# Performance work log

Hardware: AMD Instinct MI355X
Metric: run time of the kernel (lower is better)

Reference implementation:

```python
import jax, jax.numpy as jnp
import numpy as np

N_HEADS = 16
EPS = 1e-4


def setup_inputs() -> dict:
    key = jax.random.key(0)
    ks = jax.random.split(key, 9)
    B, L, E = 4, 4096, 1024
    s = 1.0 / np.sqrt(E)
    return {
        "x": jax.random.normal(ks[0], (B, L, E), dtype=jnp.float32),
        "Wq": jax.random.normal(ks[1], (E, E), dtype=jnp.float32) * s,
        "bq": jax.random.normal(ks[2], (E,), dtype=jnp.float32) * 0.01,
        "Wk": jax.random.normal(ks[3], (E, E), dtype=jnp.float32) * s,
        "bk": jax.random.normal(ks[4], (E,), dtype=jnp.float32) * 0.01,
        "Wv": jax.random.normal(ks[5], (E, E), dtype=jnp.float32) * s,
        "bv": jax.random.normal(ks[6], (E,), dtype=jnp.float32) * 0.01,
        "Wo": jax.random.normal(ks[7], (E, E), dtype=jnp.float32) * s,
        "bo": jax.random.normal(ks[8], (E,), dtype=jnp.float32) * 0.01,
    }


def _cosformer(x, Wq, bq, Wk, bk, Wv, bv, Wo, bo):
    B, L, E = x.shape
    H = N_HEADS
    hd = E // H
    # torch Linear: y = x @ W.T + b; self-attention so q=k=v source is x
    q = jax.nn.relu(jnp.einsum('ble,fe->blf', x, Wq) + bq)
    k = jax.nn.relu(jnp.einsum('ble,fe->blf', x, Wk) + bk)
    v = jnp.einsum('ble,fe->blf', x, Wv) + bv
    # (B, L, E) -> (B*H, L, hd)  [matches torch view(L, B*H, hd).transpose(0,1)]
    def split_heads(t):
        return t.reshape(B, L, H, hd).transpose(0, 2, 1, 3).reshape(B * H, L, hd)
    q, k, v = split_heads(q), split_heads(k), split_heads(v)
    m = L  # src_len == tgt_len
    idx = (np.pi / 2) * jnp.arange(1, m + 1, dtype=jnp.float32) / m  # (m,)
    sin = jnp.sin(idx)[None, :, None]
    cos = jnp.cos(idx)[None, :, None]
    q_ = jnp.concatenate([q * sin, q * cos], axis=-1)  # (BH, L, 2hd)
    k_ = jnp.concatenate([k * sin, k * cos], axis=-1)
    kv = jnp.einsum('nld,nlm->ndm', k_, v)             # (BH, 2hd, hd)
    z = 1.0 / jnp.maximum(jnp.einsum('nld,nd->nl', q_, k_.sum(axis=1)), EPS)
    attn = jnp.einsum('nld,ndm->nlm', q_, kv) * z[:, :, None]  # (BH, L, hd)
    # (B*H, L, hd) -> (B, L, E)
    out = attn.reshape(B, H, L, hd).transpose(0, 2, 1, 3).reshape(B, L, E)
    return jnp.einsum('ble,fe->blf', out, Wo) + bo


def reference(x, Wq, bq, Wk, bk, Wv, bv, Wo, bo):
    return _cosformer(x, Wq, bq, Wk, bk, Wv, bv, Wo, bo)
```

## Files before the change

### kernel.cpp

```cpp
#include <hip/hip_runtime.h>


typedef unsigned short u16;
typedef unsigned int u32;
typedef __attribute__((ext_vector_type(8))) __bf16 bf16x8;
typedef __attribute__((ext_vector_type(4))) float f32x4;

#define PI_HALF 1.57079632679489662f
#define EPS_Z 1e-4f

__device__ __forceinline__ u16 f32_to_bf16(float f) {
    union { float f; unsigned int u; } x; x.f = f;
    unsigned int lsb = (x.u >> 16) & 1u;
    x.u += 0x7fffu + lsb;
    return (u16)(x.u >> 16);
}
__device__ __forceinline__ float bf16_to_f32(u16 u) {
    union { float f; unsigned int u; } x; x.u = ((unsigned int)u) << 16;
    return x.f;
}

typedef __attribute__((address_space(1))) void amdgpu_global_t;
typedef __attribute__((address_space(3))) void amdgpu_lds_t;
__device__ __forceinline__ void async_load16(const u16* g, u16* l) {
    __builtin_amdgcn_global_load_lds((amdgpu_global_t*)g, (amdgpu_lds_t*)l, 16, 0, 0);
}

__global__ __launch_bounds__(256) void cvt_bf16(const float* __restrict__ in,
                                                u16* __restrict__ out, int n4) {
    int i = blockIdx.x * 256 + threadIdx.x;
    if (i >= n4) return;
    float4 f = ((const float4*)in)[i];
    ushort4 o;
    o.x = f32_to_bf16(f.x); o.y = f32_to_bf16(f.y);
    o.z = f32_to_bf16(f.z); o.w = f32_to_bf16(f.w);
    ((ushort4*)out)[i] = o;
}

__global__ __launch_bounds__(256) void cvt_w4(const float* __restrict__ w0,
                                              const float* __restrict__ w1,
                                              const float* __restrict__ w2,
                                              const float* __restrict__ w3,
                                              u16* __restrict__ wcat) {
    const float* src = (blockIdx.y == 0) ? w0 : (blockIdx.y == 1) ? w1
                     : (blockIdx.y == 2) ? w2 : w3;
    u16* dst = wcat + (size_t)blockIdx.y * 1048576;
    int i = blockIdx.x * 256 + threadIdx.x;
    float4 f = ((const float4*)src)[i];
    ushort4 o;
    o.x = f32_to_bf16(f.x); o.y = f32_to_bf16(f.y);
    o.z = f32_to_bf16(f.z); o.w = f32_to_bf16(f.w);
    ((ushort4*)dst)[i] = o;
}

__global__ __launch_bounds__(256) void gemm_qkv(const u16* __restrict__ A,
                                                const u16* __restrict__ Wcat,
                                                const float* __restrict__ bq,
                                                const float* __restrict__ bk,
                                                const float* __restrict__ bv,
                                                u16* __restrict__ qo,
                                                u16* __restrict__ ko,
                                                u16* __restrict__ vo) {
    __shared__ u16 As[128 * 32];
    __shared__ u16 Bs[128 * 32];
    const int K = 1024;
    const int tid  = threadIdx.x;
    const int wave = tid >> 6;
    const int lane = tid & 63;
    const int quad = lane >> 4;
    const int l15  = lane & 15;
    const long tileM = (long)blockIdx.x * 128;
    const long tileN = (long)blockIdx.y * 128;
    const int mat = blockIdx.y >> 3;
    const float* bias = (mat == 0) ? bq : (mat == 1) ? bk : bv;
    u16* outp = (mat == 0) ? qo : (mat == 1) ? ko : vo;
    const bool relu = (mat < 2);
    const int wm = (wave >> 1) * 64;
    const int wn = (wave & 1) * 64;
    const int s_row = wave * 32 + (lane >> 2);
    const int s_col = (lane & 3) * 8;

    const u16* gA = A    + (tileM + s_row) * (long)K + s_col;
    const u16* gB = Wcat + (tileN + s_row) * (long)K + s_col;
    u16* lA = &As[wave * 1024];
    u16* lB = &Bs[wave * 1024];

    f32x4 acc[4][4] = {};

    for (int kb = 0; kb < K; kb += 32) {
        async_load16(gA,                lA);
        async_load16(gA + 16 * (long)K, lA + 512);
        async_load16(gB,                lB);
        async_load16(gB + 16 * (long)K, lB + 512);
        gA += 32; gB += 32;
        __syncthreads();
        bf16x8 af[4], bf[4];
#pragma unroll
        for (int i = 0; i < 4; i++) {
            af[i] = *(const bf16x8*)&As[(wm + i * 16 + l15) * 32 + quad * 8];
            bf[i] = *(const bf16x8*)&Bs[(wn + i * 16 + l15) * 32 + quad * 8];
        }
#pragma unroll
        for (int i = 0; i < 4; i++)
#pragma unroll
            for (int j = 0; j < 4; j++)
                acc[i][j] = __builtin_amdgcn_mfma_f32_16x16x32_bf16(
                    af[i], bf[j], acc[i][j], 0, 0, 0);
        __syncthreads();
    }

#pragma unroll
    for (int j = 0; j < 4; j++) {
        const long n = tileN + wn + j * 16 + l15;
        const int nl = (int)n & 1023;
        const float bv_ = bias[nl];
#pragma unroll
        for (int i = 0; i < 4; i++) {
            const long m0 = tileM + wm + i * 16 + quad * 4;
#pragma unroll
            for (int r = 0; r < 4; r++) {
                float v = acc[i][j][r] + bv_;
                if (relu) v = fmaxf(v, 0.0f);
                outp[(m0 + r) * 1024 + nl] = f32_to_bf16(v);
            }
        }
    }
}

__global__ __launch_bounds__(256) void gemm_o(const u16* __restrict__ A,
                                              const u16* __restrict__ Bw,
                                              const float* __restrict__ bias,
                                              float* __restrict__ Cout,
                                              int M, int N, int K) {
    __shared__ u16 As[128 * 32];
    __shared__ u16 Bs[128 * 32];
    const int tid  = threadIdx.x;
    const int wave = tid >> 6;
    const int lane = tid & 63;
    const int quad = lane >> 4;
    const int l15  = lane & 15;
    const long tileM = (long)blockIdx.x * 128;
    const long tileN = (long)blockIdx.y * 128;
    const int wm = (wave >> 1) * 64;
    const int wn = (wave & 1) * 64;
    const int s_row = wave * 32 + (lane >> 2);
    const int s_col = (lane & 3) * 8;

    const u16* gA = A  + (tileM + s_row) * (long)K + s_col;
    const u16* gB = Bw + (tileN + s_row) * (long)K + s_col;
    u16* lA = &As[wave * 1024];
    u16* lB = &Bs[wave * 1024];

    f32x4 acc[4][4] = {};

    for (int kb = 0; kb < K; kb += 32) {
        async_load16(gA,                lA);
        async_load16(gA + 16 * (long)K, lA + 512);
        async_load16(gB,                lB);
        async_load16(gB + 16 * (long)K, lB + 512);
        gA += 32; gB += 32;
        __syncthreads();
        bf16x8 af[4], bf[4];
#pragma unroll
        for (int i = 0; i < 4; i++) {
            af[i] = *(const bf16x8*)&As[(wm + i * 16 + l15) * 32 + quad * 8];
            bf[i] = *(const bf16x8*)&Bs[(wn + i * 16 + l15) * 32 + quad * 8];
        }
#pragma unroll
        for (int i = 0; i < 4; i++)
#pragma unroll
            for (int j = 0; j < 4; j++)
                acc[i][j] = __builtin_amdgcn_mfma_f32_16x16x32_bf16(
                    af[i], bf[j], acc[i][j], 0, 0, 0);
        __syncthreads();
    }

#pragma unroll
    for (int j = 0; j < 4; j++) {
        const long n = tileN + wn + j * 16 + l15;
        const float bv = bias[n];
#pragma unroll
        for (int i = 0; i < 4; i++) {
            const long m0 = tileM + wm + i * 16 + quad * 4;
#pragma unroll
            for (int r = 0; r < 4; r++)
                Cout[(m0 + r) * (long)N + n] = acc[i][j][r] + bv;
        }
    }
}

__global__ __launch_bounds__(256) void kv_mfma(const u16* __restrict__ kmat,
                                               const u16* __restrict__ vmat,
                                               float* __restrict__ part) {
    __shared__ u16 Ak[64 * 40];
    __shared__ u16 Bv[64 * 40];
    const int tid = threadIdx.x;
    const int wave = tid >> 6, lane = tid & 63;
    const int quad = lane >> 4, l15 = lane & 15;
    const int head = blockIdx.y;
    const int b = head >> 4, h = head & 15;
    const int l0 = blockIdx.x * 512;
    const int sl = tid >> 3;
    const int sc8 = tid & 7;
    const int scol = sl ^ ((sc8 & 3) << 3);
    const int krow_base = (wave & 1) * 32;
    const bool use_cos = (wave >> 1) != 0;
    const int mbase = wave * 32;

    float sv[8], cv[8];
#pragma unroll
    for (int e = 0; e < 8; e++) {
        float ang = (PI_HALF / 4096.0f) * (float)(l0 + quad * 8 + e + 1);
        sv[e] = sinf(ang); cv[e] = cosf(ang);
    }
    const float cD = 0.9999247018391445f;
    const float sD = 0.0122715382857199f;

    bf16x8 onesf;
#pragma unroll
    for (int e = 0; e < 8; e++)
        onesf[e] = (l15 == 0) ? (__bf16)1.0f : (__bf16)0.0f;

    f32x4 acc[2][5] = {};

    for (int kt = 0; kt < 16; kt++) {
        const long row = ((long)b * 4096 + l0 + kt * 32 + sl) * 1024 + h * 64 + sc8 * 8;
        uint4 kk = *(const uint4*)(kmat + row);
        uint4 vv = *(const uint4*)(vmat + row);
        const u16* kp = (const u16*)&kk;
        const u16* vp = (const u16*)&vv;
#pragma unroll
        for (int e = 0; e < 8; e++) {
            const int d = sc8 * 8 + e;
            Ak[d * 40 + scol] = kp[e];
            Bv[d * 40 + scol] = vp[e];
        }
        __syncthreads();

        bf16x8 af[2];
#pragma unroll
        for (int i = 0; i < 2; i++) {
            const int d = krow_base + i * 16 + l15;
            const int q2 = (quad ^ ((d >> 3) & 3)) * 8;
            bf16x8 raw = *(const bf16x8*)&Ak[d * 40 + q2];
            bf16x8 sc;
#pragma unroll
            for (int e = 0; e < 8; e++)
                sc[e] = (__bf16)((float)raw[e] * (use_cos ? cv[e] : sv[e]));
            af[i] = sc;
        }
        bf16x8 bfr[5];
#pragma unroll
        for (int j = 0; j < 4; j++) {
            const int n = j * 16 + l15;
            const int q2 = (quad ^ ((n >> 3) & 3)) * 8;
            bfr[j] = *(const bf16x8*)&Bv[n * 40 + q2];
        }
        bfr[4] = onesf;
#pragma unroll
        for (int i = 0; i < 2; i++)
#pragma unroll
            for (int j = 0; j < 5; j++)
                acc[i][j] = __builtin_amdgcn_mfma_f32_16x16x32_bf16(
                    af[i], bfr[j], acc[i][j], 0, 0, 0);

#pragma unroll
        for (int e = 0; e < 8; e++) {
            const float ns = sv[e] * cD + cv[e] * sD;
            cv[e] = cv[e] * cD - sv[e] * sD;
            sv[e] = ns;
        }
        __syncthreads();
    }

    float* op = part + ((long)blockIdx.x * 64 + head) * 10240;
#pragma unroll
    for (int i = 0; i < 2; i++)
#pragma unroll
        for (int j = 0; j < 5; j++)
#pragma unroll
            for (int r = 0; r < 4; r++)
                op[(mbase + i * 16 + quad * 4 + r) * 80 + j * 16 + l15] = acc[i][j][r];
}

__global__ __launch_bounds__(256) void kv_reduce_t(const float* __restrict__ part,
                                                   u16* __restrict__ Bt) {
    __shared__ float accs[32 * 81];
    const int head = blockIdx.y, d2t = blockIdx.x;
    const float* bp = part + (long)head * 10240 + d2t * 32 * 80;
    for (int idx = threadIdx.x; idx < 2560; idx += 256) {
        float s = 0.0f;
#pragma unroll
        for (int c = 0; c < 8; c++) s += bp[(long)c * 655360 + idx];
        const int d2 = idx / 80, n = idx - d2 * 80;
        accs[d2 * 81 + n] = s;
    }
    __syncthreads();
    for (int idx = threadIdx.x; idx < 2560; idx += 256) {
        const int n = idx >> 5, d2 = idx & 31;
        Bt[(long)head * 10240 + n * 128 + d2t * 32 + d2] = f32_to_bf16(accs[d2 * 81 + n]);
    }
}

__global__ __launch_bounds__(256) void attn_mfma(const u16* __restrict__ qb,
                                                 const u16* __restrict__ Bt,
                                                 u16* __restrict__ merged) {
    __shared__ __align__(16) u16 As[128 * 72];
    __shared__ __align__(16) u16 Bs[80 * 136];
    const int tid = threadIdx.x;
    const int wave = tid >> 6, lane = tid & 63;
    const int quad = lane >> 4, l15 = lane & 15;
    const int head = blockIdx.y;
    const int b = head >> 4, h = head & 15;
    const int tm = blockIdx.x * 128;
    const long b4 = (long)b * 4096;

    for (int c = tid; c < 1024; c += 256) {
        const int row = c >> 3, c8 = c & 7;
        uint4 t = *(const uint4*)(qb + (b4 + tm + row) * 1024 + h * 64 + c8 * 8);
        *(uint4*)&As[row * 72 + c8 * 8] = t;
    }
    for (int c = tid; c < 1280; c += 256) {
        const int row = c >> 4, c16 = c & 15;
        uint4 t = *(const uint4*)(Bt + (long)head * 10240 + row * 128 + c16 * 8);
        *(uint4*)&Bs[row * 136 + c16 * 8] = t;
    }
    const int wm = wave * 32;
    float snl[2], csl[2];
#pragma unroll
    for (int i = 0; i < 2; i++) {
        const int l = tm + wm + i * 16 + l15;
        const float idx = PI_HALF * (float)(l + 1) * (1.0f / 4096.0f);
        snl[i] = sinf(idx); csl[i] = cosf(idx);
    }
    __syncthreads();

    f32x4 acc[2][5] = {};
#pragma unroll
    for (int kb = 0; kb < 4; kb++) {
        const int qc = (kb & 1) * 32 + quad * 8;
        bf16x8 af[2];
#pragma unroll
        for (int i = 0; i < 2; i++) {
            bf16x8 raw = *(const bf16x8*)&As[(wm + i * 16 + l15) * 72 + qc];
            const float s = (kb < 2) ? snl[i] : csl[i];
            bf16x8 sc;
#pragma unroll
            for (int e = 0; e < 8; e++) sc[e] = (__bf16)((float)raw[e] * s);
            af[i] = sc;
        }
        bf16x8 bf[5];
#pragma unroll
        for (int j = 0; j < 5; j++)
            bf[j] = *(const bf16x8*)&Bs[(j * 16 + l15) * 136 + kb * 32 + quad * 8];
#pragma unroll
        for (int i = 0; i < 2; i++)
#pragma unroll
            for (int j = 0; j < 5; j++)
                acc[i][j] = __builtin_amdgcn_mfma_f32_16x16x32_bf16(
                    af[i], bf[j], acc[i][j], 0, 0, 0);
    }

#pragma unroll
    for (int i = 0; i < 2; i++) {
        float z[4];
#pragma unroll
        for (int r = 0; r < 4; r++) {
            const float den = __shfl(acc[i][4][r], lane & 0x30, 64);
            z[r] = 1.0f / fmaxf(den, EPS_Z);
        }
#pragma unroll
        for (int j = 0; j < 4; j++)
#pragma unroll
            for (int r = 0; r < 4; r++) {
                const int l = tm + wm + i * 16 + quad * 4 + r;
                merged[(b4 + l) * 1024 + h * 64 + j * 16 + l15] =
                    f32_to_bf16(acc[i][j][r] * z[r]);
            }
    }
}

extern "C" void kernel_launch(void* const* d_in, const int* in_sizes, int n_in,
                              void* d_out, int out_size, void* d_ws, size_t ws_size,
                              hipStream_t stream) {
    (void)in_sizes; (void)n_in; (void)out_size; (void)ws_size;
    const float* x  = (const float*)d_in[0];
    const float* Wq = (const float*)d_in[1];
    const float* bq = (const float*)d_in[2];
    const float* Wk = (const float*)d_in[3];
    const float* bk = (const float*)d_in[4];
    const float* Wv = (const float*)d_in[5];
    const float* bv = (const float*)d_in[6];
    const float* Wo = (const float*)d_in[7];
    const float* bo = (const float*)d_in[8];
    float* out = (float*)d_out;

    const int M = 16384, E = 1024;
    char* ws = (char*)d_ws;
    const size_t MB = 1048576;
    u16* xb   = (u16*)(ws);
    u16* qb   = (u16*)(ws + 32 * MB);
    u16* kb   = (u16*)(ws + 64 * MB);
    u16* vb   = (u16*)(ws + 96 * MB);
    u16* wcat = (u16*)(ws + 128 * MB);
    u16* wob  = wcat + 3 * (size_t)E * E;
    u16* Btb  = (u16*)(ws + 136 * MB);
    float* part = (float*)xb;
    u16* mergedb = kb;

    cvt_bf16<<<dim3(M * E / 4 / 256), dim3(256), 0, stream>>>(x, xb, M * E / 4);
    cvt_w4<<<dim3(E * E / 4 / 256, 4), dim3(256), 0, stream>>>(Wq, Wk, Wv, Wo, wcat);

    gemm_qkv<<<dim3(M / 128, 24), dim3(256), 0, stream>>>(xb, wcat, bq, bk, bv,
                                                          qb, kb, vb);

    kv_mfma<<<dim3(8, 64), dim3(256), 0, stream>>>(kb, vb, part);
    kv_reduce_t<<<dim3(4, 64), dim3(256), 0, stream>>>(part, Btb);
    attn_mfma<<<dim3(32, 64), dim3(256), 0, stream>>>(qb, Btb, mergedb);

    gemm_o<<<dim3(M / 128, E / 128), dim3(256), 0, stream>>>(mergedb, wob, bo,
                                                             out, M, E, E);
}
```

Before: 378.7 us.

## Rewrite QKV and output GEMMs with 256x256 tiles and double-buffered LDS pipeline

Replaces the 128x128 single-buffered GEMM kernels with a shared 256x256 tile core using 512 threads, 64-wide K steps, XOR-swizzled LDS layout, and double-buffered async global-to-LDS prefetch two stages ahead. MFMA work is interleaved with LDS fragment reads and barriers, with wave priority raised around the MFMA bursts, and the block index is swizzled for L2 locality. The goal is more data reuse per tile, less LDS bank conflict, and load latency hidden behind compute. In exchange each block uses far more LDS (128 KB) and registers, so fewer blocks fit per CU and the grid is much smaller (256 blocks for the output GEMM).

```diff
diff --git a/kernel.cpp b/kernel.cpp
--- a/kernel.cpp
+++ b/kernel.cpp
@@ -53,138 +53,185 @@
     ((ushort4*)dst)[i] = o;
 }
 
-__global__ __launch_bounds__(256) void gemm_qkv(const u16* __restrict__ A,
-                                                const u16* __restrict__ Wcat,
-                                                const float* __restrict__ bq,
-                                                const float* __restrict__ bk,
-                                                const float* __restrict__ bv,
-                                                u16* __restrict__ qo,
-                                                u16* __restrict__ ko,
-                                                u16* __restrict__ vo) {
-    __shared__ u16 As[128 * 32];
-    __shared__ u16 Bs[128 * 32];
-    const int K = 1024;
+__device__ __forceinline__ void gemm256_core(const u16* __restrict__ Abase,
+                                             const u16* __restrict__ Bbase,
+                                             u16* As, u16* Bs,
+                                             f32x4 (&acc)[8][4]) {
     const int tid  = threadIdx.x;
     const int wave = tid >> 6;
     const int lane = tid & 63;
     const int quad = lane >> 4;
     const int l15  = lane & 15;
-    const long tileM = (long)blockIdx.x * 128;
-    const long tileN = (long)blockIdx.y * 128;
-    const int mat = blockIdx.y >> 3;
+    const int wr   = wave >> 2;
+    const int wc   = wave & 3;
+    const int srow = tid >> 3;
+    const int scg  = (tid & 7) ^ (srow & 7);
+
+    const u16* Ag = Abase + ((long)srow << 10) + scg * 8;
+    const u16* Bg = Bbase + ((long)srow << 10) + scg * 8;
+
+    auto stage = [&](const u16* g, u16* lb, int hs, int t) {
+        async_load16(g + ((long)hs << 16) + (t << 6), lb + hs * 4096);
+    };
+    auto rdA = [&](const u16* buf, int mf, int kk) -> bf16x8 {
+        const int R = wr * 128 + mf * 16 + l15;
+        return *(const bf16x8*)(buf + R * 64 + ((kk * 32 + quad * 8) ^ ((R & 7) * 8)));
+    };
+    auto rdB = [&](const u16* buf, int nf, int kk) -> bf16x8 {
+        const int R = wc * 64 + nf * 16 + l15;
+        return *(const bf16x8*)(buf + R * 64 + ((kk * 32 + quad * 8) ^ ((R & 7) * 8)));
+    };
+
+    bf16x8 a[4][2], b[4][2];
+    auto mfma8 = [&](int i0, int j0) {
+        __builtin_amdgcn_s_setprio(1);
+#pragma unroll
+        for (int i = 0; i < 4; ++i)
+#pragma unroll
+            for (int j = 0; j < 2; ++j)
+#pragma unroll
+                for (int kk = 0; kk < 2; ++kk)
+                    acc[i0 + i][j0 + j] = __builtin_amdgcn_mfma_f32_16x16x32_bf16(
+                        a[i][kk], b[j0 + j][kk], acc[i0 + i][j0 + j], 0, 0, 0);
+        __builtin_amdgcn_s_setprio(0);
+    };
+
+#pragma unroll
+    for (int hs = 0; hs < 4; ++hs) stage(Ag, As + wave * 512, hs, 0);
+#pragma unroll
+    for (int hs = 0; hs < 4; ++hs) stage(Bg, Bs + wave * 512, hs, 0);
+#pragma unroll
+    for (int hs = 0; hs < 4; ++hs) stage(Ag, As + 16384 + wave * 512, hs, 1);
+#pragma unroll
+    for (int hs = 0; hs < 4; ++hs) stage(Bg, Bs + 16384 + wave * 512, hs, 1);
+    asm volatile("s_waitcnt vmcnt(8)" ::: "memory");
+    __builtin_amdgcn_s_barrier();
+
+#pragma unroll 1
+    for (int t = 0; t < 16; ++t) {
+        const int cur = t & 1;
+        const u16* Ab = As + cur * 16384;
+        const u16* Bb = Bs + cur * 16384;
+        u16* lA = As + cur * 16384 + wave * 512;
+        u16* lB = Bs + cur * 16384 + wave * 512;
+        const bool pf = (t < 14);
+
+#pragma unroll
+        for (int i = 0; i < 4; ++i) { a[i][0] = rdA(Ab, i, 0); a[i][1] = rdA(Ab, i, 1); }
+#pragma unroll
+        for (int j = 0; j < 2; ++j) { b[j][0] = rdB(Bb, j, 0); b[j][1] = rdB(Bb, j, 1); }
+        __builtin_amdgcn_s_barrier();
+        asm volatile("s_waitcnt lgkmcnt(0)" ::: "memory");
+        mfma8(0, 0);
+        __builtin_amdgcn_s_barrier();
+
+#pragma unroll
+        for (int j = 2; j < 4; ++j) { b[j][0] = rdB(Bb, j, 0); b[j][1] = rdB(Bb, j, 1); }
+        __builtin_amdgcn_s_barrier();
+        asm volatile("s_waitcnt lgkmcnt(0)" ::: "memory");
+        mfma8(0, 2);
+        __builtin_amdgcn_s_barrier();
+        asm volatile("" ::: "memory");
+
+#pragma unroll
+        for (int i = 0; i < 4; ++i) { a[i][0] = rdA(Ab, i + 4, 0); a[i][1] = rdA(Ab, i + 4, 1); }
+        if (pf) {
+#pragma unroll
+            for (int hs = 0; hs < 4; ++hs) stage(Bg, lB, hs, t + 2);
+        }
+        __builtin_amdgcn_s_barrier();
+        asm volatile("s_waitcnt lgkmcnt(0)" ::: "memory");
+        mfma8(4, 0);
+        __builtin_amdgcn_s_barrier();
+        asm volatile("" ::: "memory");
+
+        if (pf) {
+#pragma unroll
+            for (int hs = 0; hs < 4; ++hs) stage(Ag, lA, hs, t + 2);
+            asm volatile("s_waitcnt vmcnt(8)" ::: "memory");
+        } else {
+            asm volatile("s_waitcnt vmcnt(0)" ::: "memory");
+        }
+        __builtin_amdgcn_s_barrier();
+        mfma8(4, 2);
+        __builtin_amdgcn_s_barrier();
+    }
+}
+
+__global__ __launch_bounds__(512, 2) void gemm_qkv(const u16* __restrict__ A,
+                                                   const u16* __restrict__ Wcat,
+                                                   const float* __restrict__ bq,
+                                                   const float* __restrict__ bk,
+                                                   const float* __restrict__ bv,
+                                                   u16* __restrict__ qo,
+                                                   u16* __restrict__ ko,
+                                                   u16* __restrict__ vo) {
+    __shared__ __align__(16) u16 As[32768];
+    __shared__ __align__(16) u16 Bs[32768];
+    const int bid = blockIdx.x;
+    const int swz = (bid & 7) * 96 + (bid >> 3);
+    const int bx  = swz / 12;
+    const int byy = swz - bx * 12;
+    const long tileM = (long)bx * 256;
+
+    f32x4 acc[8][4] = {};
+    gemm256_core(A + (tileM << 10), Wcat + ((long)byy << 18), As, Bs, acc);
+
+    const int wave = (int)threadIdx.x >> 6;
+    const int lane = (int)threadIdx.x & 63;
+    const int quad = lane >> 4, l15 = lane & 15;
+    const int wr = wave >> 2, wc = wave & 3;
+    const int mat = byy >> 2;
     const float* bias = (mat == 0) ? bq : (mat == 1) ? bk : bv;
     u16* outp = (mat == 0) ? qo : (mat == 1) ? ko : vo;
     const bool relu = (mat < 2);
-    const int wm = (wave >> 1) * 64;
-    const int wn = (wave & 1) * 64;
-    const int s_row = wave * 32 + (lane >> 2);
-    const int s_col = (lane & 3) * 8;
-
-    const u16* gA = A    + (tileM + s_row) * (long)K + s_col;
-    const u16* gB = Wcat + (tileN + s_row) * (long)K + s_col;
-    u16* lA = &As[wave * 1024];
-    u16* lB = &Bs[wave * 1024];
-
-    f32x4 acc[4][4] = {};
-
-    for (int kb = 0; kb < K; kb += 32) {
-        async_load16(gA,                lA);
-        async_load16(gA + 16 * (long)K, lA + 512);
-        async_load16(gB,                lB);
-        async_load16(gB + 16 * (long)K, lB + 512);
-        gA += 32; gB += 32;
-        __syncthreads();
-        bf16x8 af[4], bf[4];
-#pragma unroll
-        for (int i = 0; i < 4; i++) {
-            af[i] = *(const bf16x8*)&As[(wm + i * 16 + l15) * 32 + quad * 8];
-            bf[i] = *(const bf16x8*)&Bs[(wn + i * 16 + l15) * 32 + quad * 8];
-        }
-#pragma unroll
-        for (int i = 0; i < 4; i++)
-#pragma unroll
-            for (int j = 0; j < 4; j++)
-                acc[i][j] = __builtin_amdgcn_mfma_f32_16x16x32_bf16(
-                    af[i], bf[j], acc[i][j], 0, 0, 0);
-        __syncthreads();
-    }
-
-#pragma unroll
-    for (int j = 0; j < 4; j++) {
-        const long n = tileN + wn + j * 16 + l15;
-        const int nl = (int)n & 1023;
-        const float bv_ = bias[nl];
-#pragma unroll
-        for (int i = 0; i < 4; i++) {
-            const long m0 = tileM + wm + i * 16 + quad * 4;
-#pragma unroll
-            for (int r = 0; r < 4; r++) {
-                float v = acc[i][j][r] + bv_;
+    const int nbase = (byy & 3) * 256 + wc * 64;
+    const long m00 = tileM + wr * 128;
+#pragma unroll
+    for (int j = 0; j < 4; ++j) {
+        const int n = nbase + j * 16 + l15;
+        const float bb = bias[n];
+#pragma unroll
+        for (int i = 0; i < 8; ++i) {
+            const long m0 = m00 + i * 16 + quad * 4;
+#pragma unroll
+            for (int r = 0; r < 4; ++r) {
+                float v = acc[i][j][r] + bb;
                 if (relu) v = fmaxf(v, 0.0f);
-                outp[(m0 + r) * 1024 + nl] = f32_to_bf16(v);
+                outp[(m0 + r) * 1024 + n] = f32_to_bf16(v);
             }
         }
     }
 }
 
-__global__ __launch_bounds__(256) void gemm_o(const u16* __restrict__ A,
-                                              const u16* __restrict__ Bw,
-                                              const float* __restrict__ bias,
-                                              float* __restrict__ Cout,
-                                              int M, int N, int K) {
-    __shared__ u16 As[128 * 32];
-    __shared__ u16 Bs[128 * 32];
-    const int tid  = threadIdx.x;
-    const int wave = tid >> 6;
-    const int lane = tid & 63;
-    const int quad = lane >> 4;
-    const int l15  = lane & 15;
-    const long tileM = (long)blockIdx.x * 128;
-    const long tileN = (long)blockIdx.y * 128;
-    const int wm = (wave >> 1) * 64;
-    const int wn = (wave & 1) * 64;
-    const int s_row = wave * 32 + (lane >> 2);
-    const int s_col = (lane & 3) * 8;
-
-    const u16* gA = A  + (tileM + s_row) * (long)K + s_col;
-    const u16* gB = Bw + (tileN + s_row) * (long)K + s_col;
-    u16* lA = &As[wave * 1024];
-    u16* lB = &Bs[wave * 1024];
-
-    f32x4 acc[4][4] = {};
-
-    for (int kb = 0; kb < K; kb += 32) {
-        async_load16(gA,                lA);
-        async_load16(gA + 16 * (long)K, lA + 512);
-        async_load16(gB,                lB);
-        async_load16(gB + 16 * (long)K, lB + 512);
-        gA += 32; gB += 32;
-        __syncthreads();
-        bf16x8 af[4], bf[4];
-#pragma unroll
-        for (int i = 0; i < 4; i++) {
-            af[i] = *(const bf16x8*)&As[(wm + i * 16 + l15) * 32 + quad * 8];
-            bf[i] = *(const bf16x8*)&Bs[(wn + i * 16 + l15) * 32 + quad * 8];
-        }
-#pragma unroll
-        for (int i = 0; i < 4; i++)
-#pragma unroll
-            for (int j = 0; j < 4; j++)
-                acc[i][j] = __builtin_amdgcn_mfma_f32_16x16x32_bf16(
-                    af[i], bf[j], acc[i][j], 0, 0, 0);
-        __syncthreads();
-    }
-
-#pragma unroll
-    for (int j = 0; j < 4; j++) {
-        const long n = tileN + wn + j * 16 + l15;
-        const float bv = bias[n];
-#pragma unroll
-        for (int i = 0; i < 4; i++) {
-            const long m0 = tileM + wm + i * 16 + quad * 4;
-#pragma unroll
-            for (int r = 0; r < 4; r++)
-                Cout[(m0 + r) * (long)N + n] = acc[i][j][r] + bv;
+__global__ __launch_bounds__(512, 2) void gemm_o(const u16* __restrict__ A,
+                                                 const u16* __restrict__ Bw,
+                                                 const float* __restrict__ bias,
+                                                 float* __restrict__ Cout) {
+    __shared__ __align__(16) u16 As[32768];
+    __shared__ __align__(16) u16 Bs[32768];
+    const int bid = blockIdx.x;
+    const int swz = (bid & 7) * 32 + (bid >> 3);
+    const long tileM = (long)(swz >> 2) * 256;
+    const long tileN = (long)(swz & 3) * 256;
+
+    f32x4 acc[8][4] = {};
+    gemm256_core(A + (tileM << 10), Bw + (tileN << 10), As, Bs, acc);
+
+    const int wave = (int)threadIdx.x >> 6;
+    const int lane = (int)threadIdx.x & 63;
+    const int quad = lane >> 4, l15 = lane & 15;
+    const int wr = wave >> 2, wc = wave & 3;
+#pragma unroll
+    for (int j = 0; j < 4; ++j) {
+        const long n = tileN + wc * 64 + j * 16 + l15;
+        const float bb = bias[n];
+#pragma unroll
+        for (int i = 0; i < 8; ++i) {
+            const long m0 = tileM + wr * 128 + i * 16 + quad * 4;
+#pragma unroll
+            for (int r = 0; r < 4; ++r)
+                Cout[(m0 + r) * 1024 + n] = acc[i][j][r] + bb;
         }
     }
 }
@@ -411,13 +458,11 @@
     cvt_bf16<<<dim3(M * E / 4 / 256), dim3(256), 0, stream>>>(x, xb, M * E / 4);
     cvt_w4<<<dim3(E * E / 4 / 256, 4), dim3(256), 0, stream>>>(Wq, Wk, Wv, Wo, wcat);
 
-    gemm_qkv<<<dim3(M / 128, 24), dim3(256), 0, stream>>>(xb, wcat, bq, bk, bv,
-                                                          qb, kb, vb);
+    gemm_qkv<<<dim3(768), dim3(512), 0, stream>>>(xb, wcat, bq, bk, bv, qb, kb, vb);
 
     kv_mfma<<<dim3(8, 64), dim3(256), 0, stream>>>(kb, vb, part);
     kv_reduce_t<<<dim3(4, 64), dim3(256), 0, stream>>>(part, Btb);
     attn_mfma<<<dim3(32, 64), dim3(256), 0, stream>>>(qb, Btb, mergedb);
 
-    gemm_o<<<dim3(M / 128, E / 128), dim3(256), 0, stream>>>(mergedb, wob, bo,
-                                                             out, M, E, E);
-}
+    gemm_o<<<dim3(256), dim3(512), 0, stream>>>(mergedb, wob, bo, out);
+}
```

Result: faster. 369.5 us (-2.4%).
